# Kernel tuning notes

Measured on AMD Instinct MI355X. Metric: run time of the kernel, lower is better.

## Reference

```python
import jax, jax.numpy as jnp
import numpy as np

IN_FEATURES = 4096
OUT_FEATURES = 4096
SPARSITY = 0.98


def _build_mask():
    # Mirrors _initialize_structured_sparsity: banded deterministic pattern.
    num_connections = int((1 - SPARSITY) * IN_FEATURES * OUT_FEATURES)
    cpn = max(1, num_connections // OUT_FEATURES)  # connections per neuron (=81)
    rows = np.arange(OUT_FEATURES)[:, None]                      # [O,1]
    cols = (rows * cpn + np.arange(cpn)[None, :]) % IN_FEATURES  # [O,cpn]
    mask = np.zeros((OUT_FEATURES, IN_FEATURES), dtype=np.float32)
    mask[np.repeat(np.arange(OUT_FEATURES), cpn), cols.reshape(-1)] = 1.0
    return mask, cpn


def setup_inputs() -> dict:
    key = jax.random.key(0)
    kx, kw = jax.random.split(key)
    mask_np, cpn = _build_mask()
    x = jax.random.normal(kx, (16384, IN_FEATURES), dtype=jnp.float32)
    # weight init: randn * sqrt(2/cpn) at masked positions (dense tensor is fine;
    # forward multiplies by mask anyway, matching the torch module exactly)
    weight = jax.random.normal(kw, (OUT_FEATURES, IN_FEATURES), dtype=jnp.float32) * jnp.float32(np.sqrt(2.0 / cpn))
    bias = jnp.zeros((OUT_FEATURES,), dtype=jnp.float32)
    mask = jnp.asarray(mask_np)
    return {"x": x, "weight": weight, "bias": bias, "mask": mask}


def reference(x, weight, bias, mask):
    # F.linear(x, weight*mask, bias) == x @ (weight*mask).T + bias
    masked_weight = weight * mask  # [O,I]
    return jnp.einsum('bi,oi->bo', x, masked_weight) + bias
```

## Files before the change

### kernel.cpp

```cpp
#include <hip/hip_runtime.h>
#include <hip/hip_bf16.h>

#define IN_F 4096
#define OUT_F 4096
#define CPN 81
#define OINV 2225
#define OB16 2832

#define BMF 8
#define NCH 8
#define CHUNK 512
#define SC4 148
#define NLD 1184
#define XSTR 616
#define RSTRF 8

typedef __attribute__((ext_vector_type(4))) float f32x4;
typedef __attribute__((ext_vector_type(8))) short bf16x8;

__device__ __forceinline__ unsigned short f2bf(float f) {
  __hip_bfloat16 h = __float2bfloat16(f);
  return *reinterpret_cast<unsigned short*>(&h);
}
__device__ __forceinline__ float bf2f(unsigned short u) {
  unsigned int v = ((unsigned int)u) << 16;
  return *reinterpret_cast<float*>(&v);
}

__global__ void prep_wfrag(const float* __restrict__ w,
                           const float* __restrict__ mask,
                           unsigned short* __restrict__ wfrag) {
  int idx = blockIdx.x * 256 + threadIdx.x;
  int lane = idx & 63;
  int t = (idx >> 6) % 3;
  int g = idx / 192;
  int n = lane & 15;
  int kg = lane >> 4;
  int s = g * 16 + n;
  int o = (OINV * s) & 4095;
  unsigned short v8[8];
#pragma unroll
  for (int i = 0; i < 8; ++i) {
    int c = 32 * t + 8 * kg + i;
    int j = c - n;
    float v = 0.f;
    if (j >= 0 && j < CPN) {
      int col = (16 * g + c) & 4095;
      v = w[(size_t)o * IN_F + col] * mask[(size_t)o * IN_F + col];
    }
    v8[i] = f2bf(v);
  }
  *reinterpret_cast<bf16x8*>(wfrag + (size_t)idx * 8) =
      *reinterpret_cast<const bf16x8*>(v8);
}

__global__ __launch_bounds__(512, 4) void sc_fused(
    const float* __restrict__ x, const float* __restrict__ bias,
    const unsigned short* __restrict__ wfrag, float* __restrict__ out) {
  __shared__ unsigned short res[4096 * RSTRF];
  __shared__ unsigned short xl[BMF * XSTR];

  const int blk = blockIdx.x;
  const int b0 = blk * BMF;
  const int tid = threadIdx.x;
  const int wave = tid >> 6;
  const int lane = tid & 63;
  const int ln = lane & 15;
  const int lk = lane >> 4;
  const int oln = (OINV * ln) & 4095;
  const int q0 = blk & 7;

  const int i1 = tid + 512, i2 = tid + 1024;
  const int row0 = tid / SC4, c40 = tid - row0 * SC4;
  const int row1 = i1  / SC4, c41 = i1  - row1 * SC4;
  const int row2 = i2  / SC4, c42 = i2  - row2 * SC4;
  const bool v2 = (i2 < NLD);
  const float* xp0 = x + (size_t)(b0 + row0) * IN_F;
  const float* xp1 = x + (size_t)(b0 + row1) * IN_F;
  const float* xp2 = x + (size_t)(b0 + row2) * IN_F;
  unsigned short* xw0 = xl + row0 * XSTR + 4 * c40;
  unsigned short* xw1 = xl + row1 * XSTR + 4 * c41;
  unsigned short* xw2 = xl + row2 * XSTR + 4 * c42;

  auto loadx = [&](int q, float4& r0, float4& r1, float4& r2) {
    const int c0 = q * CHUNK;
    r0 = *reinterpret_cast<const float4*>(xp0 + ((c0 + 4 * c40) & 4095));
    r1 = *reinterpret_cast<const float4*>(xp1 + ((c0 + 4 * c41) & 4095));
    if (v2) r2 = *reinterpret_cast<const float4*>(xp2 + ((c0 + 4 * c42) & 4095));
  };
  auto drain = [&](const float4& r0, const float4& r1, const float4& r2) {
    ushort4 h;
    h.x = f2bf(r0.x); h.y = f2bf(r0.y); h.z = f2bf(r0.z); h.w = f2bf(r0.w);
    *reinterpret_cast<ushort4*>(xw0) = h;
    h.x = f2bf(r1.x); h.y = f2bf(r1.y); h.z = f2bf(r1.z); h.w = f2bf(r1.w);
    *reinterpret_cast<ushort4*>(xw1) = h;
    if (v2) {
      h.x = f2bf(r2.x); h.y = f2bf(r2.y); h.z = f2bf(r2.z); h.w = f2bf(r2.w);
      *reinterpret_cast<ushort4*>(xw2) = h;
    }
  };
  auto grp = [&](int g, const unsigned short* ap,
                 bf16x8 b0f, bf16x8 b1f, bf16x8 b2f) {
    bf16x8 a0 = *reinterpret_cast<const bf16x8*>(ap);
    bf16x8 a1 = *reinterpret_cast<const bf16x8*>(ap + 32);
    bf16x8 a2 = *reinterpret_cast<const bf16x8*>(ap + 64);
    f32x4 acc = f32x4{0.f, 0.f, 0.f, 0.f};
    acc = __builtin_amdgcn_mfma_f32_16x16x32_bf16(a0, b0f, acc, 0, 0, 0);
    acc = __builtin_amdgcn_mfma_f32_16x16x32_bf16(a1, b1f, acc, 0, 0, 0);
    acc = __builtin_amdgcn_mfma_f32_16x16x32_bf16(a2, b2f, acc, 0, 0, 0);
    if (lk < 2) {
      int o = (OB16 * g + oln) & 4095;
      ushort4 h;
      h.x = f2bf(acc[0]); h.y = f2bf(acc[1]);
      h.z = f2bf(acc[2]); h.w = f2bf(acc[3]);
      *reinterpret_cast<ushort4*>(res + o * RSTRF + 4 * lk) = h;
    }
  };
  auto compute = [&](int q) {
    const int gbase = q * 32 + wave * 4;
    const bf16x8* wf = reinterpret_cast<const bf16x8*>(wfrag)
                     + (size_t)gbase * 192 + lane;
    bf16x8 w0 = wf[0],   w1 = wf[64],  w2  = wf[128];
    bf16x8 w3 = wf[192], w4 = wf[256], w5  = wf[320];
    bf16x8 w6 = wf[384], w7 = wf[448], w8  = wf[512];
    bf16x8 w9 = wf[576], w10 = wf[640], w11 = wf[704];
    const unsigned short* ap = xl + (ln & 7) * XSTR + 8 * lk + 16 * (wave * 4);
    grp(gbase + 0, ap,      w0, w1, w2);
    grp(gbase + 1, ap + 16, w3, w4, w5);
    grp(gbase + 2, ap + 32, w6, w7, w8);
    grp(gbase + 3, ap + 48, w9, w10, w11);
  };

  float4 xA0, xA1, xA2, xB0, xB1, xB2;
  loadx(q0, xA0, xA1, xA2);

  for (int qq = 0; qq < NCH; qq += 2) {
    const int qa = (q0 + qq) & 7;
    const int qb = (q0 + qq + 1) & 7;

    loadx(qb, xB0, xB1, xB2);
    __builtin_amdgcn_sched_barrier(0);
    drain(xA0, xA1, xA2);
    __syncthreads();
    compute(qa);
    __syncthreads();

    if (qq + 2 < NCH) {
      loadx((q0 + qq + 2) & 7, xA0, xA1, xA2);
      __builtin_amdgcn_sched_barrier(0);
    }
    drain(xB0, xB1, xB2);
    __syncthreads();
    compute(qb);
    __syncthreads();
  }

  const int j  = lane & 3;
  const int ol = lane >> 2;
#pragma unroll 4
  for (int it = 0; it < 32; ++it) {
    int o = it * 128 + wave * 16 + ol;
    unsigned int v = *reinterpret_cast<const unsigned int*>(res + o * RSTRF + 2 * j);
    float b = bias[o];
    float lo = bf2f((unsigned short)(v & 0xffff)) + b;
    float hi = bf2f((unsigned short)(v >> 16)) + b;
    size_t base = (size_t)(b0 + 2 * j) * OUT_F + o;
    out[base]         = lo;
    out[base + OUT_F] = hi;
  }
}

extern "C" void kernel_launch(void* const* d_in, const int* in_sizes, int n_in,
                              void* d_out, int out_size, void* d_ws, size_t ws_size,
                              hipStream_t stream) {
  const float* x    = (const float*)d_in[0];
  const float* w    = (const float*)d_in[1];
  const float* bias = (const float*)d_in[2];
  const float* mask = (const float*)d_in[3];
  float* out = (float*)d_out;

  unsigned short* wfrag = (unsigned short*)d_ws;

  const int B = in_sizes[0] / IN_F;

  prep_wfrag<<<192, 256, 0, stream>>>(w, mask, wfrag);
  sc_fused<<<B / BMF, 512, 0, stream>>>(x, bias, wfrag, out);
}
```

Baseline: 159.0 us.

## Double-buffer x chunks in LDS and halve the K-chunk size

Splits the input row into 16 chunks of 256 columns instead of 8 chunks of 512, and keeps two LDS buffers for x. While one chunk is used for MFMA compute, the next chunk is converted to bf16 and written into the other buffer. This leaves one barrier per chunk instead of two. Each wave now handles two 16-column groups per chunk rather than four, so there are more loop iterations, each with less work and fewer weight registers held.

```diff
diff --git a/kernel.cpp b/kernel.cpp
--- a/kernel.cpp
+++ b/kernel.cpp
@@ -8,11 +8,11 @@
 #define OB16 2832
 
 #define BMF 8
-#define NCH 8
-#define CHUNK 512
-#define SC4 148
-#define NLD 1184
-#define XSTR 616
+#define NCH 16
+#define CHUNK 256
+#define SC4 84
+#define NLD 672
+#define XSTR 344
 #define RSTRF 8
 
 typedef __attribute__((ext_vector_type(4))) float f32x4;
@@ -58,7 +58,7 @@
     const float* __restrict__ x, const float* __restrict__ bias,
     const unsigned short* __restrict__ wfrag, float* __restrict__ out) {
   __shared__ unsigned short res[4096 * RSTRF];
-  __shared__ unsigned short xl[BMF * XSTR];
+  __shared__ unsigned short xl[2][BMF * XSTR];
 
   const int blk = blockIdx.x;
   const int b0 = blk * BMF;
@@ -68,35 +68,29 @@
   const int ln = lane & 15;
   const int lk = lane >> 4;
   const int oln = (OINV * ln) & 4095;
-  const int q0 = blk & 7;
+  const int q0 = blk & 15;
 
-  const int i1 = tid + 512, i2 = tid + 1024;
+  const int i1 = tid + 512;
   const int row0 = tid / SC4, c40 = tid - row0 * SC4;
-  const int row1 = i1  / SC4, c41 = i1  - row1 * SC4;
-  const int row2 = i2  / SC4, c42 = i2  - row2 * SC4;
-  const bool v2 = (i2 < NLD);
+  const int row1 = i1 / SC4,  c41 = i1 - row1 * SC4;
+  const bool v1 = (i1 < NLD);
   const float* xp0 = x + (size_t)(b0 + row0) * IN_F;
   const float* xp1 = x + (size_t)(b0 + row1) * IN_F;
-  const float* xp2 = x + (size_t)(b0 + row2) * IN_F;
-  unsigned short* xw0 = xl + row0 * XSTR + 4 * c40;
-  unsigned short* xw1 = xl + row1 * XSTR + 4 * c41;
-  unsigned short* xw2 = xl + row2 * XSTR + 4 * c42;
+  const int xo0 = row0 * XSTR + 4 * c40;
+  const int xo1 = row1 * XSTR + 4 * c41;
 
-  auto loadx = [&](int q, float4& r0, float4& r1, float4& r2) {
+  auto loadx = [&](int q, float4& r0, float4& r1) {
     const int c0 = q * CHUNK;
     r0 = *reinterpret_cast<const float4*>(xp0 + ((c0 + 4 * c40) & 4095));
-    r1 = *reinterpret_cast<const float4*>(xp1 + ((c0 + 4 * c41) & 4095));
-    if (v2) r2 = *reinterpret_cast<const float4*>(xp2 + ((c0 + 4 * c42) & 4095));
+    if (v1) r1 = *reinterpret_cast<const float4*>(xp1 + ((c0 + 4 * c41) & 4095));
   };
-  auto drain = [&](const float4& r0, const float4& r1, const float4& r2) {
+  auto drain = [&](int buf, const float4& r0, const float4& r1) {
     ushort4 h;
     h.x = f2bf(r0.x); h.y = f2bf(r0.y); h.z = f2bf(r0.z); h.w = f2bf(r0.w);
-    *reinterpret_cast<ushort4*>(xw0) = h;
-    h.x = f2bf(r1.x); h.y = f2bf(r1.y); h.z = f2bf(r1.z); h.w = f2bf(r1.w);
-    *reinterpret_cast<ushort4*>(xw1) = h;
-    if (v2) {
-      h.x = f2bf(r2.x); h.y = f2bf(r2.y); h.z = f2bf(r2.z); h.w = f2bf(r2.w);
-      *reinterpret_cast<ushort4*>(xw2) = h;
+    *reinterpret_cast<ushort4*>(&xl[buf][xo0]) = h;
+    if (v1) {
+      h.x = f2bf(r1.x); h.y = f2bf(r1.y); h.z = f2bf(r1.z); h.w = f2bf(r1.w);
+      *reinterpret_cast<ushort4*>(&xl[buf][xo1]) = h;
     }
   };
   auto grp = [&](int g, const unsigned short* ap,
@@ -116,42 +110,37 @@
       *reinterpret_cast<ushort4*>(res + o * RSTRF + 4 * lk) = h;
     }
   };
-  auto compute = [&](int q) {
-    const int gbase = q * 32 + wave * 4;
+  auto compute = [&](int q, int buf) {
+    const int gbase = q * 16 + wave * 2;
     const bf16x8* wf = reinterpret_cast<const bf16x8*>(wfrag)
                      + (size_t)gbase * 192 + lane;
-    bf16x8 w0 = wf[0],   w1 = wf[64],  w2  = wf[128];
-    bf16x8 w3 = wf[192], w4 = wf[256], w5  = wf[320];
-    bf16x8 w6 = wf[384], w7 = wf[448], w8  = wf[512];
-    bf16x8 w9 = wf[576], w10 = wf[640], w11 = wf[704];
-    const unsigned short* ap = xl + (ln & 7) * XSTR + 8 * lk + 16 * (wave * 4);
+    bf16x8 w0 = wf[0],   w1 = wf[64],  w2 = wf[128];
+    bf16x8 w3 = wf[192], w4 = wf[256], w5 = wf[320];
+    const unsigned short* ap = &xl[buf][(ln & 7) * XSTR + 8 * lk + 32 * wave];
     grp(gbase + 0, ap,      w0, w1, w2);
     grp(gbase + 1, ap + 16, w3, w4, w5);
-    grp(gbase + 2, ap + 32, w6, w7, w8);
-    grp(gbase + 3, ap + 48, w9, w10, w11);
   };
 
-  float4 xA0, xA1, xA2, xB0, xB1, xB2;
-  loadx(q0, xA0, xA1, xA2);
+  float4 A0, A1, B0, B1;
+  loadx(q0, A0, A1);
+  drain(0, A0, A1);
+  loadx((q0 + 1) & 15, B0, B1);
+  __syncthreads();
 
-  for (int qq = 0; qq < NCH; qq += 2) {
-    const int qa = (q0 + qq) & 7;
-    const int qb = (q0 + qq + 1) & 7;
+  for (int i = 0; i < NCH; i += 2) {
+    const int qa = (q0 + i) & 15;
+    const int qb = (q0 + i + 1) & 15;
 
-    loadx(qb, xB0, xB1, xB2);
+    if (i + 2 < NCH) loadx((q0 + i + 2) & 15, A0, A1);
     __builtin_amdgcn_sched_barrier(0);
-    drain(xA0, xA1, xA2);
-    __syncthreads();
-    compute(qa);
+    drain(1, B0, B1);
+    compute(qa, 0);
     __syncthreads();
 
-    if (qq + 2 < NCH) {
-      loadx((q0 + qq + 2) & 7, xA0, xA1, xA2);
-      __builtin_amdgcn_sched_barrier(0);
-    }
-    drain(xB0, xB1, xB2);
-    __syncthreads();
-    compute(qb);
+    if (i + 3 < NCH) loadx((q0 + i + 3) & 15, B0, B1);
+    __builtin_amdgcn_sched_barrier(0);
+    if (i + 2 < NCH) drain(0, A0, A1);
+    compute(qb, 1);
     __syncthreads();
   }
 
```

New measurement: 176.0 us. +10.7%, slower.
